# Performance work log

Hardware: AMD Instinct MI355X
Metric: run time of the kernel (lower is better)

The kernel has to match this reference:

```python
import math
import jax, jax.numpy as jnp
import numpy as np

B, S, D, QK, H = 4, 4096, 1024, 128, 2048  # hidden = int(2.0 * dim)
NUM_BUCKETS, MAX_DIST = 32, 128
LN_EPS = 1e-5


def setup_inputs() -> dict:
    key = jax.random.key(0)
    ks = jax.random.split(key, 7)
    x = jax.random.normal(ks[0], (B, S, D), jnp.float32)
    ln_g = jnp.ones((D,), jnp.float32)
    ln_b = jnp.zeros((D,), jnp.float32)
    Wh = jax.random.normal(ks[1], (D, 2 * H), jnp.float32) * 0.02
    bh = jnp.zeros((2 * H,), jnp.float32)
    Wqk = jax.random.normal(ks[2], (D, QK), jnp.float32) * 0.02
    bqk = jnp.zeros((QK,), jnp.float32)
    os_gamma = jax.random.normal(ks[3], (2, QK), jnp.float32) * 0.02  # nn.init.normal_(std=0.02)
    os_beta = jnp.zeros((2, QK), jnp.float32)
    Wo = jax.random.normal(ks[4], (H, D), jnp.float32) * 0.02
    bo = jnp.zeros((D,), jnp.float32)
    rel_emb = jax.random.normal(ks[5], (NUM_BUCKETS, 1), jnp.float32) * 0.02
    return {"x": x, "ln_g": ln_g, "ln_b": ln_b, "Wh": Wh, "bh": bh,
            "Wqk": Wqk, "bqk": bqk, "os_gamma": os_gamma, "os_beta": os_beta,
            "Wo": Wo, "bo": bo, "rel_emb": rel_emb}


def _t5_rel_bias(rel_emb, seq_len, scale):
    # non-causal T5 relative position bucket (num_buckets halved to 16)
    pos = jnp.arange(seq_len)
    rel = pos[None, :] - pos[:, None]  # k_pos - q_pos -> [i, j]
    n = -rel
    nb = NUM_BUCKETS // 2  # 16
    me = nb // 2           # max_exact = 8
    ret = (n < 0).astype(jnp.int32) * nb
    na = jnp.abs(n)
    val_large = me + (jnp.log(jnp.maximum(na, 1).astype(jnp.float32) / me)
                      / math.log(MAX_DIST / me) * (nb - me)).astype(jnp.int32)
    val_large = jnp.minimum(val_large, nb - 1)
    bucket = ret + jnp.where(na < me, na, val_large)  # [S, S] in [0, 31]
    return rel_emb[bucket, 0] * scale  # [S, S]


def reference(x, ln_g, ln_b, Wh, bh, Wqk, bqk, os_gamma, os_beta, Wo, bo, rel_emb):
    seq_len = x.shape[-2]
    # LayerNorm
    mu = jnp.mean(x, axis=-1, keepdims=True)
    var = jnp.mean(jnp.square(x - mu), axis=-1, keepdims=True)
    normed = (x - mu) * jax.lax.rsqrt(var + LN_EPS) * ln_g + ln_b
    # hidden (v, gate) with SiLU
    hidden = jax.nn.silu(normed @ Wh + bh)  # [B, S, 2H]
    v, gate = hidden[..., :H], hidden[..., H:]
    # qk projection + offset/scale into q, k
    qk = jax.nn.silu(normed @ Wqk + bqk)  # [B, S, QK]
    q = qk * os_gamma[0] + os_beta[0]
    k = qk * os_gamma[1] + os_beta[1]
    sim = jnp.einsum('bid,bjd->bij', q, k)  # [B, S, S]
    sim = sim + _t5_rel_bias(rel_emb, seq_len, float(D) ** 0.5)
    attn = jnp.square(jax.nn.relu(sim / seq_len))  # ReLU^2, no softmax
    out = jnp.einsum('bij,bjd->bid', attn, v) * gate  # [B, S, H]
    out = out @ Wo + bo
    return out + x  # add_residual
```

## Files before the change

### kernel.cpp

```cpp
#include <hip/hip_runtime.h>
#include <hip/hip_bf16.h>
#include <math.h>

typedef __bf16 bf16_t;
typedef __bf16 bf16x8 __attribute__((ext_vector_type(8)));
typedef __bf16 bf16x4 __attribute__((ext_vector_type(4)));
typedef float  f32x4  __attribute__((ext_vector_type(4)));

#define S_LEN 4096
#define D_DIM 1024
#define QK_DIM 128
#define H_DIM 2048
#define BATCH 4

__device__ __forceinline__ void gld_lds16(const void* g, void* l) {
  __builtin_amdgcn_global_load_lds((const __attribute__((address_space(1))) void*)g,
                                   (__attribute__((address_space(3))) void*)l, 16, 0, 0);
}

__device__ __forceinline__ float silu_f(float v) {
  return v / (1.0f + __expf(-v));
}

__device__ __forceinline__ float ldf(const void* p, size_t i, int f32) {
  return f32 ? ((const float*)p)[i] : (float)((const bf16_t*)p)[i];
}

__global__ void probe_k(const unsigned* __restrict__ ln_g_raw, int* __restrict__ flag) {
  if (threadIdx.x == 0) flag[0] = (ln_g_raw[0] == 0x3F800000u) ? 1 : 0;
}

#define M_HID 0
#define M_QK 1
#define M_SCORE 2
#define M_PV 3
#define M_OUT 4

template <int MODE>
__global__ __launch_bounds__(512)
void gemm8p(const bf16_t* __restrict__ A, const bf16_t* __restrict__ Bt, int K,
            const void* e0, const void* e1, const float* __restrict__ ef,
            void* o0, void* o1, const int* __restrict__ dflag)
{
  constexpr int BMv = (MODE == M_PV) ? 128 : 256;
  constexpr int MR  = BMv / 32;
  constexpr int MH  = MR / 2;
  constexpr int AL  = BMv / 128;
  constexpr int ATILE = BMv * 128;
  constexpr int AHALF = ATILE / 2;

  __shared__ __align__(16) char lds[2 * ATILE + 2 * 32768];
  char* const ldsA = lds;
  char* const ldsB = lds + 2 * ATILE;

  const int t = threadIdx.x;
  const int w = t >> 6, lane = t & 63;
  const int quad = lane >> 4, col = lane & 15;
  const int wm = (w >> 2) * (BMv / 2);
  const int wn = (w & 3) * 64;

  const int gx = gridDim.x;
  const int nwg = gx * (int)gridDim.y;
  const int orig = (int)blockIdx.y * gx + (int)blockIdx.x;
  const int wg = (orig & 7) * (nwg >> 3) + (orig >> 3);
  const int bx = wg & (gx - 1), by = wg >> __builtin_ctz(gx);
  const int m0 = bx * BMv, n0 = by * 256;

  const bf16_t* const Ap = A + (size_t)m0 * K;
  const bf16_t* const Bp = Bt + (size_t)n0 * K;

  int aoff[AL], boff[2];
#pragma unroll
  for (int c = 0; c < AL; ++c) {
    const int P = c * 8192 + t * 16;
    const int L = P ^ (((P >> 7) & 7) << 4);
    aoff[c] = (L >> 7) * K + ((L & 127) >> 1);
  }
#pragma unroll
  for (int c = 0; c < 2; ++c) {
    const int P = c * 8192 + t * 16;
    const int L = P ^ (((P >> 7) & 7) << 4);
    boff[c] = (L >> 7) * K + ((L & 127) >> 1);
  }

  const int xrq = (quad ^ (col & 7)) << 4;
  const int abase = (wm + col) * 128 + xrq;
  const int bbase = (wn + col) * 128 + xrq;

  f32x4 acc[MR][4] = {};
  bf16x8 aF[MH][2], b0[2][2], b1[2][2];

#define SB() __builtin_amdgcn_sched_barrier(0)
#define BAR() do { SB(); __builtin_amdgcn_s_barrier(); SB(); } while (0)

#define RD_A(mhalf) do {                                                       \
    const char* as_ = ldsA + buf * ATILE;                                      \
    _Pragma("unroll") for (int mi = 0; mi < MH; ++mi)                          \
    _Pragma("unroll") for (int s = 0; s < 2; ++s)                              \
      aF[mi][s] = *(const bf16x8*)(as_ +                                       \
          ((abase + ((mhalf) * MH + mi) * 2048) ^ (s << 6)));                  \
  } while (0)

#define RD_B(dst, nhalf) do {                                                  \
    const char* bs_ = ldsB + buf * 32768;                                      \
    _Pragma("unroll") for (int ni = 0; ni < 2; ++ni)                           \
    _Pragma("unroll") for (int s = 0; s < 2; ++s)                              \
      dst[ni][s] = *(const bf16x8*)(bs_ +                                      \
          ((bbase + ((nhalf) * 2 + ni) * 2048) ^ (s << 6)));                   \
  } while (0)

#define MM(mhalf, nhalf, BF) do {                                              \
    __builtin_amdgcn_s_setprio(1);                                             \
    _Pragma("unroll") for (int mi = 0; mi < MH; ++mi)                          \
    _Pragma("unroll") for (int ni = 0; ni < 2; ++ni)                           \
    _Pragma("unroll") for (int s = 0; s < 2; ++s)                              \
      acc[(mhalf) * MH + mi][(nhalf) * 2 + ni] =                               \
        __builtin_amdgcn_mfma_f32_16x16x32_bf16(                               \
            aF[mi][s], BF[ni][s], acc[(mhalf) * MH + mi][(nhalf) * 2 + ni],    \
            0, 0, 0);                                                          \
    __builtin_amdgcn_s_setprio(0);                                             \
  } while (0)

#define STG_A(tt) do {                                                         \
    char* base_ = ldsA + ((tt) & 1) * ATILE + w * 1024;                        \
    const bf16_t* g_ = Ap + (size_t)(tt) * 64;                                 \
    _Pragma("unroll") for (int h_ = 0; h_ < 2; ++h_)                           \
    _Pragma("unroll") for (int c_ = 0; c_ < AL; ++c_)                          \
      gld_lds16(g_ + (size_t)(h_ * (BMv / 2)) * K + aoff[c_],                  \
                base_ + h_ * AHALF + c_ * 8192);                               \
  } while (0)

#define STG_B(tt, h) do {                                                      \
    char* base_ = ldsB + ((tt) & 1) * 32768 + (h) * 16384 + w * 1024;          \
    const bf16_t* g_ = Bp + (size_t)((h) * 128) * K + (size_t)(tt) * 64;       \
    _Pragma("unroll") for (int c_ = 0; c_ < 2; ++c_)                           \
      gld_lds16(g_ + boff[c_], base_ + c_ * 8192);                             \
  } while (0)

#define WAIT_STEADY() do {                                                     \
    if constexpr (AL == 2) asm volatile("s_waitcnt vmcnt(4)" ::: "memory");    \
    else                   asm volatile("s_waitcnt vmcnt(2)" ::: "memory");    \
  } while (0)

  const int NT = K >> 6;

  STG_A(0); STG_B(0, 0); STG_B(0, 1); STG_A(1);
  WAIT_STEADY();
  BAR();

  for (int tt = 0; tt < NT; ++tt) {
    const int buf = tt & 1;
    RD_A(0); RD_B(b0, 0);
    if (tt + 1 < NT) STG_B(tt + 1, 0);
    BAR();
    MM(0, 0, b0);
    BAR();
    RD_B(b1, 1);
    if (tt + 1 < NT) STG_B(tt + 1, 1);
    BAR();
    MM(0, 1, b1);
    BAR();
    RD_A(1);
    BAR();
    MM(1, 1, b1);
    BAR();
    if (tt + 2 < NT) STG_A(tt + 2);
    BAR();
    MM(1, 0, b0);
    SB();
    if (tt + 1 < NT) {
      if (tt + 2 < NT) WAIT_STEADY();
      else asm volatile("s_waitcnt vmcnt(0)" ::: "memory");
    }
    BAR();
  }

#undef SB
#undef BAR
#undef RD_A
#undef RD_B
#undef MM
#undef STG_A
#undef STG_B
#undef WAIT_STEADY

  __syncthreads();

  int f32 = 0;
  if constexpr (MODE == M_HID || MODE == M_OUT) f32 = dflag[0];

  if constexpr (MODE == M_OUT) {
    float (*swzf)[16][68] = (float (*)[16][68])lds;
#pragma unroll
    for (int m = 0; m < MR; ++m) {
#pragma unroll
      for (int j = 0; j < 4; ++j)
#pragma unroll
        for (int r = 0; r < 4; ++r)
          swzf[w][quad * 4 + r][j * 16 + col] = acc[m][j][r];
#pragma unroll
      for (int it = 0; it < 4; ++it) {
        const int task = it * 64 + lane, gr = task >> 4, ch = task & 15;
        const int gm = m0 + wm + m * 16 + gr;
        const int gnc = n0 + wn + ch * 4;
        f32x4 vv = *(const f32x4*)&swzf[w][gr][ch * 4];
        float xr4[4], r4[4];
        if (f32) {
          float4 t4 = *(const float4*)((const float*)e1 + (size_t)gm * D_DIM + gnc);
          xr4[0] = t4.x; xr4[1] = t4.y; xr4[2] = t4.z; xr4[3] = t4.w;
        } else {
          bf16x4 t4 = *(const bf16x4*)((const bf16_t*)e1 + (size_t)gm * D_DIM + gnc);
#pragma unroll
          for (int qq = 0; qq < 4; ++qq) xr4[qq] = (float)t4[qq];
        }
#pragma unroll
        for (int qq = 0; qq < 4; ++qq)
          r4[qq] = vv[qq] + ldf(e0, gnc + qq, f32) + xr4[qq];
        if (f32) {
          float4 s4 = {r4[0], r4[1], r4[2], r4[3]};
          *(float4*)((float*)o0 + (size_t)gm * D_DIM + gnc) = s4;
        } else {
          bf16x4 s4;
#pragma unroll
          for (int qq = 0; qq < 4; ++qq) s4[qq] = (bf16_t)r4[qq];
          *(bf16x4*)((bf16_t*)o0 + (size_t)gm * D_DIM + gnc) = s4;
        }
      }
    }
    return;
  }

  if constexpr (MODE == M_HID) {
    if (n0 < H_DIM) {
      bf16_t (*swzT)[16][136] = (bf16_t (*)[16][136])lds;
      const int bb  = m0 >> 12;
      const int smb = (m0 + wm) & (S_LEN - 1);
#pragma unroll
      for (int j = 0; j < 4; ++j) {
        const int gnj = n0 + wn + j * 16;
        const float bhv = ldf(e0, gnj + col, f32);
#pragma unroll
        for (int m = 0; m < MR; ++m)
#pragma unroll
          for (int r = 0; r < 4; ++r)
            swzT[w][col][m * 16 + quad * 4 + r] = (bf16_t)silu_f(acc[m][j][r] + bhv);
#pragma unroll
        for (int it = 0; it < 4; ++it) {
          const int task = it * 64 + lane, gr = task >> 4, ch = task & 15;
          bf16x8 vv = *(const bf16x8*)&swzT[w][gr][ch * 8];
          const size_t off = ((size_t)bb * H_DIM + (gnj + gr)) * S_LEN + smb + ch * 8;
          *(bf16x8*)((bf16_t*)o0 + off) = vv;
        }
      }
      return;
    }
  }

  if constexpr (MODE == M_HID || MODE == M_SCORE || MODE == M_PV) {
    bf16_t (*swzb)[16][72] = (bf16_t (*)[16][72])lds;
#pragma unroll
    for (int m = 0; m < MR; ++m) {
#pragma unroll
      for (int j = 0; j < 4; ++j) {
        const int gn = n0 + wn + j * 16 + col;
#pragma unroll
        for (int r = 0; r < 4; ++r) {
          const float val = acc[m][j][r];
          bf16_t sv;
          if constexpr (MODE == M_HID) {
            sv = (bf16_t)silu_f(val + ldf(e0, gn, f32));
          } else if constexpr (MODE == M_SCORE) {
            const int gm = m0 + wm + m * 16 + quad * 4 + r;
            float wgt = fmaxf((val + ef[gm - gn + (S_LEN - 1)]) *
                              (1.0f / (float)S_LEN), 0.0f);
            sv = (bf16_t)(wgt * wgt);
          } else {
            sv = (bf16_t)val;
          }
          swzb[w][quad * 4 + r][j * 16 + col] = sv;
        }
      }
#pragma unroll
      for (int it = 0; it < 2; ++it) {
        const int task = it * 64 + lane, gr = task >> 3, ch = task & 7;
        const int gm  = m0 + wm + m * 16 + gr;
        const int gnb = n0 + wn + ch * 8;
        bf16x8 vv = *(const bf16x8*)&swzb[w][gr][ch * 8];
        if constexpr (MODE == M_HID) {
          *(bf16x8*)((bf16_t*)o1 + (size_t)gm * H_DIM + (gnb - H_DIM)) = vv;
        } else if constexpr (MODE == M_SCORE) {
          *(bf16x8*)((bf16_t*)o0 + (size_t)gm * S_LEN + gnb) = vv;
        } else {
          bf16x8 g8 = *(const bf16x8*)((const bf16_t*)e0 + (size_t)gm * H_DIM + gnb);
          bf16x8 r8;
#pragma unroll
          for (int qq = 0; qq < 8; ++qq)
            r8[qq] = (bf16_t)((float)vv[qq] * (float)g8[qq]);
          *(bf16x8*)((bf16_t*)o0 + (size_t)gm * H_DIM + gnb) = r8;
        }
      }
    }
  }
}

template <int MODE>
__global__ __launch_bounds__(256)
void gemm_bt(const bf16_t* __restrict__ A, const bf16_t* __restrict__ Bt,
             int M, int N, int K,
             const void* e0, const void* e1, const void* e2,
             const float* __restrict__ ef,
             void* o0, void* o1, const int* __restrict__ dflag)
{
  __shared__ __align__(16) bf16_t As[128 * 32];
  __shared__ __align__(16) bf16_t Bs[128 * 32];
  const int t = threadIdx.x;
  const int w = t >> 6, lane = t & 63;
  const int quad = lane >> 4, col = lane & 15;
  const int wm = (w >> 1) << 6, wn = (w & 1) << 6;
  const int m0 = blockIdx.x * 128, n0 = blockIdx.y * 128;
  const int f32 = dflag[0];

  f32x4 acc[4][4] = {};

  for (int k0 = 0; k0 < K; k0 += 32) {
    __syncthreads();
    for (int p = 0; p < 2; ++p) {
      const int chunk = w * 2 + p;
      const int fl = (chunk * 64 + lane) * 8;
      const int r = fl >> 5, c = fl & 31;
      gld_lds16(A  + (size_t)(m0 + r) * K + (k0 + c), &As[chunk * 512]);
      gld_lds16(Bt + (size_t)(n0 + r) * K + (k0 + c), &Bs[chunk * 512]);
    }
    __syncthreads();

    bf16x8 af[4], bfr[4];
#pragma unroll
    for (int i = 0; i < 4; ++i)
      af[i] = *(const bf16x8*)&As[(wm + i * 16 + col) * 32 + quad * 8];
#pragma unroll
    for (int i = 0; i < 4; ++i)
      bfr[i] = *(const bf16x8*)&Bs[(wn + i * 16 + col) * 32 + quad * 8];
#pragma unroll
    for (int i = 0; i < 4; ++i)
#pragma unroll
      for (int j = 0; j < 4; ++j)
        acc[i][j] = __builtin_amdgcn_mfma_f32_16x16x32_bf16(af[i], bfr[j], acc[i][j], 0, 0, 0);
  }

#pragma unroll
  for (int i = 0; i < 4; ++i) {
#pragma unroll
    for (int j = 0; j < 4; ++j) {
#pragma unroll
      for (int r = 0; r < 4; ++r) {
        const int gm = m0 + wm + i * 16 + quad * 4 + r;
        const int gn = n0 + wn + j * 16 + col;
        float val = acc[i][j][r] + ldf(e0, gn, f32);
        float s = silu_f(val);
        ((bf16_t*)o0)[(size_t)gm * QK_DIM + gn] =
            (bf16_t)(s * ldf(e1, gn, f32) + ldf(e2, gn, f32));
        ((bf16_t*)o1)[(size_t)gm * QK_DIM + gn] =
            (bf16_t)(s * ldf(e1, QK_DIM + gn, f32) + ldf(e2, QK_DIM + gn, f32));
      }
    }
  }
}

__global__ __launch_bounds__(256)
void layernorm_k(const void* __restrict__ x, const void* __restrict__ g,
                 const void* __restrict__ be, bf16_t* __restrict__ out,
                 const int* __restrict__ dflag)
{
  const int row = blockIdx.x;
  const int t = threadIdx.x;
  const int f32 = dflag[0];
  float f[4];
  if (f32) {
    const float* xr = (const float*)x + (size_t)row * D_DIM;
    float4 xv = *(const float4*)&xr[t * 4];
    f[0] = xv.x; f[1] = xv.y; f[2] = xv.z; f[3] = xv.w;
  } else {
    const bf16_t* xr = (const bf16_t*)x + (size_t)row * D_DIM;
    bf16x4 xv = *(const bf16x4*)&xr[t * 4];
#pragma unroll
    for (int i = 0; i < 4; ++i) f[i] = (float)xv[i];
  }
  float s = 0.f, sq = 0.f;
#pragma unroll
  for (int i = 0; i < 4; ++i) { s += f[i]; sq += f[i] * f[i]; }
#pragma unroll
  for (int off = 32; off > 0; off >>= 1) {
    s += __shfl_down(s, off);
    sq += __shfl_down(sq, off);
  }
  __shared__ float red[8];
  const int w = t >> 6;
  if ((t & 63) == 0) { red[w] = s; red[4 + w] = sq; }
  __syncthreads();
  s = red[0] + red[1] + red[2] + red[3];
  sq = red[4] + red[5] + red[6] + red[7];
  const float mu = s * (1.0f / D_DIM);
  const float var = sq * (1.0f / D_DIM) - mu * mu;
  const float inv = rsqrtf(var + 1e-5f);
  bf16x4 ov;
#pragma unroll
  for (int i = 0; i < 4; ++i) {
    float nv = (f[i] - mu) * inv * ldf(g, t * 4 + i, f32) + ldf(be, t * 4 + i, f32);
    ov[i] = (bf16_t)nv;
  }
  *(bf16x4*)&out[(size_t)row * D_DIM + t * 4] = ov;
}

__global__ __launch_bounds__(256)
void transpose_k(const void* __restrict__ src, bf16_t* __restrict__ dst,
                 int R, int C, const int* __restrict__ dflag)
{
  __shared__ bf16_t tile[32][33];
  const int f32 = dflag[0];
  const int c0 = blockIdx.x * 32, r0 = blockIdx.y * 32;
  for (int i = threadIdx.y; i < 32; i += 8)
    tile[i][threadIdx.x] = (bf16_t)ldf(src, (size_t)(r0 + i) * C + (c0 + threadIdx.x), f32);
  __syncthreads();
  for (int i = threadIdx.y; i < 32; i += 8)
    dst[(size_t)(c0 + i) * R + (r0 + threadIdx.x)] = tile[threadIdx.x][i];
}

__global__ void bias_k(const void* __restrict__ rel_emb, float* __restrict__ bias,
                       const int* __restrict__ dflag)
{
  int d = blockIdx.x * 256 + threadIdx.x;
  if (d >= 2 * S_LEN - 1) return;
  const int f32 = dflag[0];
  int n = d - (S_LEN - 1);
  int ret = (n < 0) ? 16 : 0;
  int na = n < 0 ? -n : n;
  int b;
  if (na < 8) b = na;
  else {
    float vl = logf((float)na * (1.0f / 8.0f)) / logf(16.0f) * 8.0f;
    int vi = 8 + (int)vl;
    b = vi > 15 ? 15 : vi;
  }
  bias[d] = ldf(rel_emb, ret + b, f32) * 32.0f;
}

extern "C" void kernel_launch(void* const* d_in, const int* in_sizes, int n_in,
                              void* d_out, int out_size, void* d_ws, size_t ws_size,
                              hipStream_t stream)
{
  const void* x    = d_in[0];
  const void* ln_g = d_in[1];
  const void* ln_b = d_in[2];
  const void* Wh   = d_in[3];
  const void* bh   = d_in[4];
  const void* Wqk  = d_in[5];
  const void* bqk  = d_in[6];
  const void* osg  = d_in[7];
  const void* osb  = d_in[8];
  const void* Wo   = d_in[9];
  const void* bo   = d_in[10];
  const void* rel  = d_in[11];

  const int BS = BATCH * S_LEN;
  char* p = (char*)d_ws;
  int*    flags  = (int*)p;     p += 256;
  float*  bias   = (float*)p;   p += (size_t)8192 * 4;
  bf16_t* WhT    = (bf16_t*)p;  p += (size_t)4096 * 1024 * 2;
  bf16_t* WqkT   = (bf16_t*)p;  p += (size_t)128 * 1024 * 2;
  bf16_t* WoT    = (bf16_t*)p;  p += (size_t)1024 * 2048 * 2;
  bf16_t* q      = (bf16_t*)p;  p += (size_t)BS * QK_DIM * 2;
  bf16_t* kk     = (bf16_t*)p;  p += (size_t)BS * QK_DIM * 2;
  bf16_t* vT     = (bf16_t*)p;  p += (size_t)BS * H_DIM * 2;
  bf16_t* gate   = (bf16_t*)p;  p += (size_t)BS * H_DIM * 2;
  bf16_t* normed = (bf16_t*)p;  p += (size_t)BS * D_DIM * 2;
  bf16_t* attn   = normed;
  bf16_t* pvg    = gate;

  probe_k<<<1, 64, 0, stream>>>((const unsigned*)ln_g, flags);
  bias_k<<<32, 256, 0, stream>>>(rel, bias, flags);
  transpose_k<<<dim3(4096 / 32, 1024 / 32), dim3(32, 8), 0, stream>>>(Wh, WhT, 1024, 4096, flags);
  transpose_k<<<dim3(128 / 32, 1024 / 32), dim3(32, 8), 0, stream>>>(Wqk, WqkT, 1024, 128, flags);
  transpose_k<<<dim3(1024 / 32, 2048 / 32), dim3(32, 8), 0, stream>>>(Wo, WoT, 2048, 1024, flags);
  layernorm_k<<<BS, 256, 0, stream>>>(x, ln_g, ln_b, normed, flags);

  gemm8p<M_HID><<<dim3(BS / 256, 4096 / 256), 512, 0, stream>>>(
      normed, WhT, 1024, bh, nullptr, nullptr, vT, gate, flags);
  gemm_bt<M_QK><<<dim3(BS / 128, 1), 256, 0, stream>>>(
      normed, WqkT, BS, QK_DIM, 1024, bqk, osg, osb, nullptr, q, kk, flags);

  for (int b = 0; b < BATCH; ++b) {
    gemm8p<M_SCORE><<<dim3(S_LEN / 256, S_LEN / 256), 512, 0, stream>>>(
        q + (size_t)b * S_LEN * QK_DIM, kk + (size_t)b * S_LEN * QK_DIM,
        QK_DIM, nullptr, nullptr, bias, attn, nullptr, flags);
    gemm8p<M_PV><<<dim3(S_LEN / 128, H_DIM / 256), 512, 0, stream>>>(
        attn, vT + (size_t)b * S_LEN * H_DIM, S_LEN,
        gate + (size_t)b * S_LEN * H_DIM, nullptr, nullptr,
        pvg + (size_t)b * S_LEN * H_DIM, nullptr, flags);
  }

  gemm8p<M_OUT><<<dim3(BS / 256, 1024 / 256), 512, 0, stream>>>(
      pvg, WoT, 2048, bo, x, nullptr, d_out, nullptr, flags);
}
```

Before: 843.4 us.

## Rewrite GEMM main loop with inline-asm LDS reads and peeled pipeline tail

Replaces compiler-generated LDS fragment loads with inline ds_read_b128 using immediate offsets and XOR-toggled base addresses for the double buffer. The main loop is peeled so the last two K-tiles run without branch checks, and explicit lgkmcnt waits are placed before the MFMA blocks. LDS is fixed at 128KB and launch_bounds gets a min-blocks hint of 2. This aims to cut address arithmetic and branch overhead and to control instruction scheduling, at the risk of stricter waits and register pressure. For PV mode the fixed 128KB LDS is larger than that mode needs.

```diff
diff --git a/kernel.cpp b/kernel.cpp
--- a/kernel.cpp
+++ b/kernel.cpp
@@ -6,6 +6,7 @@
 typedef __bf16 bf16x8 __attribute__((ext_vector_type(8)));
 typedef __bf16 bf16x4 __attribute__((ext_vector_type(4)));
 typedef float  f32x4  __attribute__((ext_vector_type(4)));
+typedef int    i32x4  __attribute__((ext_vector_type(4)));
 
 #define S_LEN 4096
 #define D_DIM 1024
@@ -22,6 +23,10 @@
   return v / (1.0f + __expf(-v));
 }
 
+__device__ __forceinline__ bf16x8 as_bf(i32x4 v) {
+  union { i32x4 a; bf16x8 b; } u; u.a = v; return u.b;
+}
+
 __device__ __forceinline__ float ldf(const void* p, size_t i, int f32) {
   return f32 ? ((const float*)p)[i] : (float)((const bf16_t*)p)[i];
 }
@@ -37,7 +42,7 @@
 #define M_OUT 4
 
 template <int MODE>
-__global__ __launch_bounds__(512)
+__global__ __launch_bounds__(512, 2)
 void gemm8p(const bf16_t* __restrict__ A, const bf16_t* __restrict__ Bt, int K,
             const void* e0, const void* e1, const float* __restrict__ ef,
             void* o0, void* o1, const int* __restrict__ dflag)
@@ -45,13 +50,12 @@
   constexpr int BMv = (MODE == M_PV) ? 128 : 256;
   constexpr int MR  = BMv / 32;
   constexpr int MH  = MR / 2;
-  constexpr int AL  = BMv / 128;
-  constexpr int ATILE = BMv * 128;
-  constexpr int AHALF = ATILE / 2;
-
-  __shared__ __align__(16) char lds[2 * ATILE + 2 * 32768];
+  constexpr int LA  = BMv / 128;
+  constexpr int AHALF = BMv * 64;
+
+  __shared__ __align__(16) char lds[131072];
   char* const ldsA = lds;
-  char* const ldsB = lds + 2 * ATILE;
+  char* const ldsB = lds + 65536;
 
   const int t = threadIdx.x;
   const int w = t >> 6, lane = t & 63;
@@ -69,9 +73,9 @@
   const bf16_t* const Ap = A + (size_t)m0 * K;
   const bf16_t* const Bp = Bt + (size_t)n0 * K;
 
-  int aoff[AL], boff[2];
-#pragma unroll
-  for (int c = 0; c < AL; ++c) {
+  int aoff[LA], boff[2];
+#pragma unroll
+  for (int c = 0; c < LA; ++c) {
     const int P = c * 8192 + t * 16;
     const int L = P ^ (((P >> 7) & 7) << 4);
     aoff[c] = (L >> 7) * K + ((L & 127) >> 1);
@@ -84,105 +88,157 @@
   }
 
   const int xrq = (quad ^ (col & 7)) << 4;
-  const int abase = (wm + col) * 128 + xrq;
-  const int bbase = (wn + col) * 128 + xrq;
+  const unsigned ldsA_i = (unsigned)(size_t)&lds[0];
+  unsigned aA0 = ldsA_i + (unsigned)((wm + col) * 128 + xrq);
+  unsigned aA1 = aA0 ^ 64u;
+  unsigned bA0 = ldsA_i + 65536u + (unsigned)((wn + col) * 128 + xrq);
+  unsigned bA1 = bA0 ^ 64u;
 
   f32x4 acc[MR][4] = {};
-  bf16x8 aF[MH][2], b0[2][2], b1[2][2];
+  i32x4 aF[MH][2], bX[2][2], bY[2][2];
 
 #define SB() __builtin_amdgcn_sched_barrier(0)
-#define BAR() do { SB(); __builtin_amdgcn_s_barrier(); SB(); } while (0)
-
-#define RD_A(mhalf) do {                                                       \
-    const char* as_ = ldsA + buf * ATILE;                                      \
-    _Pragma("unroll") for (int mi = 0; mi < MH; ++mi)                          \
-    _Pragma("unroll") for (int s = 0; s < 2; ++s)                              \
-      aF[mi][s] = *(const bf16x8*)(as_ +                                       \
-          ((abase + ((mhalf) * MH + mi) * 2048) ^ (s << 6)));                  \
-  } while (0)
-
-#define RD_B(dst, nhalf) do {                                                  \
-    const char* bs_ = ldsB + buf * 32768;                                      \
-    _Pragma("unroll") for (int ni = 0; ni < 2; ++ni)                           \
-    _Pragma("unroll") for (int s = 0; s < 2; ++s)                              \
-      dst[ni][s] = *(const bf16x8*)(bs_ +                                      \
-          ((bbase + ((nhalf) * 2 + ni) * 2048) ^ (s << 6)));                   \
-  } while (0)
-
-#define MM(mhalf, nhalf, BF) do {                                              \
+#define BARR() do { SB(); __builtin_amdgcn_s_barrier(); SB(); } while (0)
+#define DSR(dst, addr, lit) \
+  asm volatile("ds_read_b128 %0, %1 offset:" #lit : "=v"(dst) : "v"(addr))
+#define WAITL0() asm volatile("s_waitcnt lgkmcnt(0)" ::: "memory")
+#define WAITV4() asm volatile("s_waitcnt vmcnt(4)" ::: "memory")
+#define WAITV2() asm volatile("s_waitcnt vmcnt(2)" ::: "memory")
+#define WAITV0() asm volatile("s_waitcnt vmcnt(0)" ::: "memory")
+#define VSTEADY() do { if constexpr (BMv == 256) WAITV4(); else WAITV2(); } while (0)
+
+#define RD_AQ0() do {                                                          \
+    DSR(aF[0][0], aA0, 0);    DSR(aF[0][1], aA1, 0);                           \
+    DSR(aF[1][0], aA0, 2048); DSR(aF[1][1], aA1, 2048);                        \
+    if constexpr (MH == 4) {                                                   \
+      DSR(aF[2][0], aA0, 4096); DSR(aF[2][1], aA1, 4096);                      \
+      DSR(aF[3][0], aA0, 6144); DSR(aF[3][1], aA1, 6144);                      \
+    }                                                                          \
+  } while (0)
+#define RD_AQ1() do {                                                          \
+    if constexpr (MH == 4) {                                                   \
+      DSR(aF[0][0], aA0, 8192);  DSR(aF[0][1], aA1, 8192);                     \
+      DSR(aF[1][0], aA0, 10240); DSR(aF[1][1], aA1, 10240);                    \
+      DSR(aF[2][0], aA0, 12288); DSR(aF[2][1], aA1, 12288);                    \
+      DSR(aF[3][0], aA0, 14336); DSR(aF[3][1], aA1, 14336);                    \
+    } else {                                                                   \
+      DSR(aF[0][0], aA0, 4096); DSR(aF[0][1], aA1, 4096);                      \
+      DSR(aF[1][0], aA0, 6144); DSR(aF[1][1], aA1, 6144);                      \
+    }                                                                          \
+  } while (0)
+#define RD_BX() do {                                                           \
+    DSR(bX[0][0], bA0, 0);    DSR(bX[0][1], bA1, 0);                           \
+    DSR(bX[1][0], bA0, 2048); DSR(bX[1][1], bA1, 2048);                        \
+  } while (0)
+#define RD_BY() do {                                                           \
+    DSR(bY[0][0], bA0, 4096); DSR(bY[0][1], bA1, 4096);                        \
+    DSR(bY[1][0], bA0, 6144); DSR(bY[1][1], bA1, 6144);                        \
+  } while (0)
+
+#define MM(mh, nh, BSET) do {                                                  \
     __builtin_amdgcn_s_setprio(1);                                             \
     _Pragma("unroll") for (int mi = 0; mi < MH; ++mi)                          \
     _Pragma("unroll") for (int ni = 0; ni < 2; ++ni)                           \
     _Pragma("unroll") for (int s = 0; s < 2; ++s)                              \
-      acc[(mhalf) * MH + mi][(nhalf) * 2 + ni] =                               \
+      acc[(mh) * MH + mi][(nh) * 2 + ni] =                                     \
         __builtin_amdgcn_mfma_f32_16x16x32_bf16(                               \
-            aF[mi][s], BF[ni][s], acc[(mhalf) * MH + mi][(nhalf) * 2 + ni],    \
-            0, 0, 0);                                                          \
+            as_bf(aF[mi][s]), as_bf(BSET[ni][s]),                              \
+            acc[(mh) * MH + mi][(nh) * 2 + ni], 0, 0, 0);                      \
     __builtin_amdgcn_s_setprio(0);                                             \
   } while (0)
 
-#define STG_A(tt) do {                                                         \
-    char* base_ = ldsA + ((tt) & 1) * ATILE + w * 1024;                        \
-    const bf16_t* g_ = Ap + (size_t)(tt) * 64;                                 \
-    _Pragma("unroll") for (int h_ = 0; h_ < 2; ++h_)                           \
-    _Pragma("unroll") for (int c_ = 0; c_ < AL; ++c_)                          \
-      gld_lds16(g_ + (size_t)(h_ * (BMv / 2)) * K + aoff[c_],                  \
-                base_ + h_ * AHALF + c_ * 8192);                               \
-  } while (0)
-
-#define STG_B(tt, h) do {                                                      \
-    char* base_ = ldsB + ((tt) & 1) * 32768 + (h) * 16384 + w * 1024;          \
+#define STG_AH(tt, h) do {                                                     \
+    char* d_ = ldsA + (((tt) & 1) << 15) + (h) * AHALF + w * 1024;             \
+    const bf16_t* g_ = Ap + (size_t)((h) * (BMv / 2)) * K + (size_t)(tt) * 64; \
+    _Pragma("unroll") for (int c_ = 0; c_ < LA; ++c_)                          \
+      gld_lds16(g_ + aoff[c_], d_ + c_ * 8192);                                \
+  } while (0)
+#define STG_BH(tt, h) do {                                                     \
+    char* d_ = ldsB + (((tt) & 1) << 15) + (h) * 16384 + w * 1024;             \
     const bf16_t* g_ = Bp + (size_t)((h) * 128) * K + (size_t)(tt) * 64;       \
-    _Pragma("unroll") for (int c_ = 0; c_ < 2; ++c_)                           \
-      gld_lds16(g_ + boff[c_], base_ + c_ * 8192);                             \
-  } while (0)
-
-#define WAIT_STEADY() do {                                                     \
-    if constexpr (AL == 2) asm volatile("s_waitcnt vmcnt(4)" ::: "memory");    \
-    else                   asm volatile("s_waitcnt vmcnt(2)" ::: "memory");    \
+    gld_lds16(g_ + boff[0], d_);                                               \
+    gld_lds16(g_ + boff[1], d_ + 8192);                                        \
   } while (0)
 
   const int NT = K >> 6;
 
-  STG_A(0); STG_B(0, 0); STG_B(0, 1); STG_A(1);
-  WAIT_STEADY();
-  BAR();
-
-  for (int tt = 0; tt < NT; ++tt) {
-    const int buf = tt & 1;
-    RD_A(0); RD_B(b0, 0);
-    if (tt + 1 < NT) STG_B(tt + 1, 0);
-    BAR();
-    MM(0, 0, b0);
-    BAR();
-    RD_B(b1, 1);
-    if (tt + 1 < NT) STG_B(tt + 1, 1);
-    BAR();
-    MM(0, 1, b1);
-    BAR();
-    RD_A(1);
-    BAR();
-    MM(1, 1, b1);
-    BAR();
-    if (tt + 2 < NT) STG_A(tt + 2);
-    BAR();
-    MM(1, 0, b0);
-    SB();
-    if (tt + 1 < NT) {
-      if (tt + 2 < NT) WAIT_STEADY();
-      else asm volatile("s_waitcnt vmcnt(0)" ::: "memory");
-    }
-    BAR();
+  STG_AH(0, 0); STG_AH(0, 1);
+  STG_BH(0, 0); STG_BH(0, 1);
+  STG_AH(1, 0); STG_AH(1, 1);
+  VSTEADY();
+  BARR();
+
+  for (int tt = 0; tt < NT - 2; ++tt) {
+    RD_AQ0(); RD_BX();
+    STG_BH(tt + 1, 0); STG_BH(tt + 1, 1);
+    BARR(); WAITL0(); SB();
+    MM(0, 0, bX);
+    BARR();
+    RD_BY();
+    BARR(); WAITL0(); SB();
+    MM(0, 1, bY);
+    BARR();
+    RD_AQ1();
+    BARR(); WAITL0(); SB();
+    STG_AH(tt + 2, 0); STG_AH(tt + 2, 1);
+    MM(1, 1, bY);
+    BARR();
+    BARR();
+    MM(1, 0, bX);
+    VSTEADY(); SB();
+    BARR();
+    aA0 ^= 32768u; aA1 ^= 32768u; bA0 ^= 32768u; bA1 ^= 32768u;
+  }
+
+  {
+    RD_AQ0(); RD_BX();
+    STG_BH(NT - 1, 0); STG_BH(NT - 1, 1);
+    BARR(); WAITL0(); SB();
+    MM(0, 0, bX);
+    BARR();
+    RD_BY();
+    BARR(); WAITL0(); SB();
+    MM(0, 1, bY);
+    BARR();
+    RD_AQ1();
+    BARR(); WAITL0(); SB();
+    MM(1, 1, bY);
+    BARR();
+    BARR();
+    MM(1, 0, bX);
+    WAITV0(); SB();
+    BARR();
+    aA0 ^= 32768u; aA1 ^= 32768u; bA0 ^= 32768u; bA1 ^= 32768u;
+    RD_AQ0(); RD_BX();
+    BARR(); WAITL0(); SB();
+    MM(0, 0, bX);
+    BARR();
+    RD_BY();
+    BARR(); WAITL0(); SB();
+    MM(0, 1, bY);
+    BARR();
+    RD_AQ1();
+    BARR(); WAITL0(); SB();
+    MM(1, 1, bY);
+    BARR();
+    MM(1, 0, bX);
   }
 
 #undef SB
-#undef BAR
-#undef RD_A
-#undef RD_B
+#undef BARR
+#undef DSR
+#undef WAITL0
+#undef WAITV4
+#undef WAITV2
+#undef WAITV0
+#undef VSTEADY
+#undef RD_AQ0
+#undef RD_AQ1
+#undef RD_BX
+#undef RD_BY
 #undef MM
-#undef STG_A
-#undef STG_B
-#undef WAIT_STEADY
+#undef STG_AH
+#undef STG_BH
 
   __syncthreads();
 
```

New measurement: 806.9 us. -4.3%, faster.
